# Optimization experiments

Hardware: AMD Instinct MI355X
Metric: run time of the kernel (lower is better)

Reference implementation:

```python
import jax, jax.numpy as jnp
import numpy as np
from jax.ops import segment_sum

N_NODES = 100_000
N_EDGES = 6_400_000
NUM_HOPS = 2
DECAY = 0.5
BC_INLET, BC_OUTLET, BC_WALL = 0.1, 0.0, 0.0


def setup_inputs() -> dict:
    key = jax.random.key(0)
    ks = jax.random.split(key, 12)
    pred = jax.random.normal(ks[0], (N_NODES,), jnp.float32)
    feats = jax.random.normal(ks[1], (N_NODES, 8), jnp.float32)
    b = jax.random.normal(ks[2], (N_NODES,), jnp.float32)
    vals = jax.random.normal(ks[3], (N_EDGES,), jnp.float32)
    ic_values = jax.random.normal(ks[4], (N_NODES,), jnp.float32)
    row_ptr = jnp.sort(jax.random.randint(ks[5], (N_NODES + 1,), 0, N_EDGES)).astype(jnp.int64)
    col_ind = jax.random.randint(ks[6], (N_EDGES,), 0, N_NODES).astype(jnp.int64)
    row_idx = jnp.sort(jax.random.randint(ks[7], (N_EDGES,), 0, N_NODES)).astype(jnp.int64)
    edge_index = jax.random.randint(ks[8], (2, N_EDGES), 0, N_NODES).astype(jnp.int64)
    ic_mask = jax.random.randint(ks[9], (N_NODES,), 0, 2) > 0
    inlet_mask = jax.random.randint(ks[10], (N_NODES,), 0, 2) > 0
    outlet_mask = jax.random.randint(ks[11], (N_NODES,), 0, 2) > 0
    wall_mask = jax.random.randint(jax.random.fold_in(key, 99), (N_NODES,), 0, 2) > 0
    return {"pred": pred, "feats": feats, "b": b, "vals": vals, "ic_values": ic_values,
            "row_ptr": row_ptr, "col_ind": col_ind, "row_idx": row_idx,
            "edge_index": edge_index, "ic_mask": ic_mask, "inlet_mask": inlet_mask,
            "outlet_mask": outlet_mask, "wall_mask": wall_mask, "epoch": 10}


def _masked_mse(pred, mask, target):
    m = mask.astype(pred.dtype)
    denom = jnp.maximum(m.sum(), 1.0)
    return jnp.sum(m * (pred - target) ** 2) / denom


def reference(pred, feats, b, vals, ic_values, row_ptr, col_ind, row_idx,
              edge_index, ic_mask, inlet_mask, outlet_mask, wall_mask, epoch):
    N = pred.shape[0]
    src, dst = edge_index[0], edge_index[1]

    # --- physics-based mesh-quality weight (edge-length-weighted gradient indicator) ---
    coords = feats[:, :2]                      # [N,2] node coordinates
    edge_len = jnp.sqrt(jnp.sum((coords[src] - coords[dst]) ** 2, axis=-1) + 1e-12)
    edge_grad = jnp.abs(pred[src] - pred[dst])
    quality = edge_len * edge_grad             # [E]
    ones_e = jnp.ones_like(quality)
    deg = jnp.maximum(segment_sum(ones_e, dst, num_segments=N), 1.0)
    w0 = 1.0 + segment_sum(quality, dst, num_segments=N) / deg
    w0 = w0 / jnp.mean(w0)

    # --- topology-aware multi-hop weight propagation ---
    w_cell = w0
    cur = w0
    for h in range(NUM_HOPS):
        cur = segment_sum(cur[src], dst, num_segments=N) / deg  # neighbor mean
        w_cell = w_cell + (DECAY ** (h + 1)) * cur

    # --- PDE residual: CSR (COO-expanded) sparse matvec ---
    Ax = segment_sum(vals * pred[col_ind], row_idx, num_segments=N)
    residual = Ax - b
    loss_pde = jnp.mean(w_cell * residual ** 2)

    # --- boundary condition losses ---
    loss_inlet = _masked_mse(pred, inlet_mask, BC_INLET)
    loss_outlet = _masked_mse(pred, outlet_mask, BC_OUTLET)
    loss_wall = _masked_mse(pred, wall_mask, BC_WALL)
    loss_bc = loss_inlet + loss_outlet + loss_wall

    # --- initial condition loss ---
    loss_ic = _masked_mse(pred, ic_mask, ic_values)

    # --- mass conservation: per-node net flux divergence ---
    flux = pred[src] - pred[dst]               # [E]
    net = segment_sum(flux, dst, num_segments=N)
    loss_cons = jnp.mean(net ** 2)

    # hierarchical adaptive lambdas reduce to 1.0 for a single forward pass
    loss_total = loss_pde + loss_bc + loss_ic + loss_cons
    return loss_total
```

## Files before the change

kernel.cpp:

```cpp
#include <hip/hip_runtime.h>

#define N_NODES 100000
#define N_EDGES 6400000

typedef unsigned long long u64;
typedef unsigned int u32;
typedef unsigned char u8;

#define QSCALE    8192.0f
#define QSCALE_INV (1.0 / 8192.0)
#define FLUXBIAS  12.0f
#define FSHIFT    26
#define CSHIFT    51

#define W_REGIONS   1024
#define EPW         6250
#define K_BUCKETS   256
#define RANGE       391
#define NPAD        100096
#define CAP         40
#define OVF_CAP     32768
#define OVB         8
#define SPLIT       8
#define CHUNK       (W_REGIONS / SPLIT)
#define AGG_BLOCKS  (K_BUCKETS * SPLIT + OVB)

#define EDGE_BLOCKS 6250
#define NBLK_NODE   391

enum { S_W0SUM = 0, S_CONS, S_IN_S, S_IN_C, S_OUT_S, S_OUT_C,
       S_WALL_S, S_WALL_C, S_IC_S, S_IC_C, S_PDE, S_NSLOT };
#define PS_STRIDE 16

__device__ __forceinline__ double wave_reduce(double v) {
    #pragma unroll
    for (int off = 32; off > 0; off >>= 1)
        v += __shfl_down(v, off, 64);
    return v;
}

__device__ __forceinline__ u64 edge_inc(float ps, float pd, float2 cs, float2 cd) {
    const float dx = cs.x - cd.x, dy = cs.y - cd.y;
    const float flux = ps - pd;
    const float q = sqrtf(dx * dx + dy * dy + 1e-12f) * fabsf(flux);
    const u64 qq = (u64)lrintf(fminf(q, 1024.0f) * QSCALE);
    const float fb = fminf(fmaxf(flux, -FLUXBIAS), FLUXBIAS) + FLUXBIAS;
    const u64 fq = (u64)lrintf(fb * QSCALE);
    return (1ull << CSHIFT) | (fq << FSHIFT) | qq;
}

__global__ __launch_bounds__(256) void shuffle_edges(
    const int* __restrict__ ei,
    u32* __restrict__ slab,
    u8* __restrict__ counts,
    u64* __restrict__ ovf,
    u32* __restrict__ ocnt)
{
    __shared__ u32 cur[K_BUCKETS];
    __shared__ u32 lslab[K_BUCKETS * CAP];
    for (int j = threadIdx.x; j < K_BUCKETS; j += 256) cur[j] = 0;
    __syncthreads();

    const int region = blockIdx.x;
    const int ebase = region * EPW;
    for (int k = threadIdx.x; k < EPW; k += 256) {
        const int e = ebase + k;
        const u32 s = (u32)ei[e];
        const u32 d = (u32)ei[N_EDGES + e];
        const u32 b = d / RANGE;
        const u32 dl = d - b * RANGE;
        const u32 pos = atomicAdd(&cur[b], 1u);
        if (pos < CAP) {
            lslab[b * CAP + pos] = (s << 9) | dl;
        } else {
            const u32 o = atomicAdd(ocnt, 1u);
            if (o < OVF_CAP) ovf[o] = ((u64)s << 32) | d;
        }
    }
    __syncthreads();
    const uint4* lsrc = (const uint4*)lslab;
    uint4* gdst = (uint4*)(slab + (size_t)region * K_BUCKETS * CAP);
    #pragma unroll
    for (int j = threadIdx.x; j < K_BUCKETS * CAP / 4; j += 256)
        gdst[j] = lsrc[j];
    for (int j = threadIdx.x; j < K_BUCKETS; j += 256)
        counts[region * K_BUCKETS + j] = (u8)min(cur[j], (u32)CAP);
}

__global__ __launch_bounds__(256) void agg_a(
    const u32* __restrict__ slab,
    const u8* __restrict__ counts,
    const u64* __restrict__ ovf,
    const u32* __restrict__ ocnt,
    const float* __restrict__ pred,
    const float* __restrict__ feats,
    u64* __restrict__ pk_part,
    u64* __restrict__ pk_ovf)
{
    if (blockIdx.x < K_BUCKETS * SPLIT) {
        __shared__ u64 acc[RANGE];
        for (int t = threadIdx.x; t < RANGE; t += 256) acc[t] = 0;
        __syncthreads();
        const int b = blockIdx.x >> 3;
        const int chunk = blockIdx.x & 7;
        const int wl = threadIdx.x >> 6, lane = threadIdx.x & 63;
        const int nbase = b * RANGE;
        for (int w = chunk * CHUNK + wl; w < (chunk + 1) * CHUNK; w += 4) {
            const int cnt = counts[w * K_BUCKETS + b];
            if (lane < cnt) {
                const u32 ent = slab[((size_t)w * K_BUCKETS + b) * CAP + lane];
                const int src = (int)(ent >> 9);
                const int dl = (int)(ent & 511u);
                const int d = nbase + dl;
                const float2 cs = *(const float2*)(feats + (size_t)src * 8);
                const float2 cd = *(const float2*)(feats + (size_t)d * 8);
                atomicAdd(&acc[dl], edge_inc(pred[src], pred[d], cs, cd));
            }
        }
        __syncthreads();
        for (int t = threadIdx.x; t < RANGE; t += 256)
            pk_part[(size_t)chunk * NPAD + nbase + t] = acc[t];
    } else {
        const int n = min((int)*ocnt, OVF_CAP);
        for (int o = (blockIdx.x - K_BUCKETS * SPLIT) * 256 + threadIdx.x;
             o < n; o += OVB * 256) {
            const u64 e = ovf[o];
            const int src = (int)(e >> 32);
            const int d = (int)(e & 0xffffffffu);
            const float2 cs = *(const float2*)(feats + (size_t)src * 8);
            const float2 cd = *(const float2*)(feats + (size_t)d * 8);
            atomicAdd(pk_ovf + d, edge_inc(pred[src], pred[d], cs, cd));
        }
    }
}

__global__ __launch_bounds__(256) void agg_hop(
    const u32* __restrict__ slab,
    const u8* __restrict__ counts,
    const u64* __restrict__ ovf,
    const u32* __restrict__ ocnt,
    const float* __restrict__ vsrc,
    float* __restrict__ hop_part,
    float* __restrict__ hop_ovf)
{
    if (blockIdx.x < K_BUCKETS * SPLIT) {
        __shared__ float acc[RANGE];
        for (int t = threadIdx.x; t < RANGE; t += 256) acc[t] = 0.0f;
        __syncthreads();
        const int b = blockIdx.x >> 3;
        const int chunk = blockIdx.x & 7;
        const int wl = threadIdx.x >> 6, lane = threadIdx.x & 63;
        const int nbase = b * RANGE;
        for (int w = chunk * CHUNK + wl; w < (chunk + 1) * CHUNK; w += 4) {
            const int cnt = counts[w * K_BUCKETS + b];
            if (lane < cnt) {
                const u32 ent = slab[((size_t)w * K_BUCKETS + b) * CAP + lane];
                atomicAdd(&acc[ent & 511u], vsrc[ent >> 9]);
            }
        }
        __syncthreads();
        for (int t = threadIdx.x; t < RANGE; t += 256)
            hop_part[(size_t)chunk * NPAD + nbase + t] = acc[t];
    } else {
        const int n = min((int)*ocnt, OVF_CAP);
        for (int o = (blockIdx.x - K_BUCKETS * SPLIT) * 256 + threadIdx.x;
             o < n; o += OVB * 256) {
            const u64 e = ovf[o];
            atomicAdd(hop_ovf + (int)(e & 0xffffffffu), vsrc[(int)(e >> 32)]);
        }
    }
}

__global__ __launch_bounds__(256) void ax_pass(
    const float* __restrict__ pred,
    const float* __restrict__ vals,
    const int* __restrict__ col_ind,
    const int* __restrict__ row_idx,
    float* __restrict__ Ax)
{
    const int stride = gridDim.x * blockDim.x;
    const unsigned lane = threadIdx.x & 63u;
    for (int e = blockIdx.x * blockDim.x + threadIdx.x; e < N_EDGES; e += stride) {
        const int r = row_idx[e];
        float av = vals[e] * pred[col_ind[e]];
        #pragma unroll
        for (int off = 1; off < 64; off <<= 1) {
            const float ov = __shfl_up(av, off, 64);
            const int   ok = __shfl_up(r,  off, 64);
            if ((int)lane >= off && ok == r) av += ov;
        }
        const int rn = __shfl_down(r, 1, 64);
        if (lane == 63u || rn != r) atomicAdd(Ax + r, av);
    }
}

__global__ __launch_bounds__(256) void edge_pass_a(
    const int* __restrict__ ei,
    const float* __restrict__ pred,
    const float* __restrict__ feats,
    const float* __restrict__ vals,
    const int* __restrict__ col_ind,
    const int* __restrict__ row_idx,
    u64* __restrict__ pk,
    float* __restrict__ Ax)
{
    const int stride = gridDim.x * blockDim.x;
    const unsigned lane = threadIdx.x & 63u;
    for (int e = blockIdx.x * blockDim.x + threadIdx.x; e < N_EDGES; e += stride) {
        const int s = ei[e];
        const int d = ei[N_EDGES + e];
        const float2 cs = *(const float2*)(feats + (size_t)s * 8);
        const float2 cd = *(const float2*)(feats + (size_t)d * 8);
        atomicAdd(pk + d, edge_inc(pred[s], pred[d], cs, cd));
        const int r = row_idx[e];
        float av = vals[e] * pred[col_ind[e]];
        #pragma unroll
        for (int off = 1; off < 64; off <<= 1) {
            const float ov = __shfl_up(av, off, 64);
            const int   ok = __shfl_up(r,  off, 64);
            if ((int)lane >= off && ok == r) av += ov;
        }
        const int rn = __shfl_down(r, 1, 64);
        if (lane == 63u || rn != r) atomicAdd(Ax + r, av);
    }
}

__global__ __launch_bounds__(256) void edge_hop(
    const int* __restrict__ ei,
    const float* __restrict__ srcval,
    float* __restrict__ accum)
{
    const int stride = gridDim.x * blockDim.x;
    for (int e = blockIdx.x * blockDim.x + threadIdx.x; e < N_EDGES; e += stride) {
        atomicAdd(accum + ei[N_EDGES + e], srcval[ei[e]]);
    }
}

__global__ __launch_bounds__(256) void node_b(
    const float* __restrict__ pred,
    const float* __restrict__ b,
    const float* __restrict__ ic_values,
    const int* __restrict__ inlet_mask,
    const int* __restrict__ outlet_mask,
    const int* __restrict__ wall_mask,
    const int* __restrict__ ic_mask,
    const u64* __restrict__ pk_part,
    const u64* __restrict__ pk_ovf,
    float* __restrict__ w0u_out,
    float* __restrict__ deg_out,
    float* __restrict__ Ax_res2,
    double* __restrict__ part_scal)
{
    const int i = blockIdx.x * blockDim.x + threadIdx.x;
    double v10[10];
    #pragma unroll
    for (int s = 0; s < 10; ++s) v10[s] = 0.0;
    if (i < N_NODES) {
        u64 v = pk_ovf[i];
        #pragma unroll
        for (int s2 = 0; s2 < SPLIT; ++s2) v += pk_part[(size_t)s2 * NPAD + i];
        const double cnt = (double)(v >> CSHIFT);
        const double qs  = (double)(v & ((1ull << FSHIFT) - 1)) * QSCALE_INV;
        const double fs  = (double)((v >> FSHIFT) & ((1ull << (CSHIFT - FSHIFT)) - 1)) * QSCALE_INV
                           - (double)FLUXBIAS * cnt;
        const float dg = fmaxf((float)cnt, 1.0f);
        deg_out[i] = dg;
        const float w = 1.0f + (float)qs / dg;
        w0u_out[i] = w;
        v10[S_W0SUM] = (double)w;
        v10[S_CONS] = fs * fs;
        const float p = pred[i];
        const float res = Ax_res2[i] - b[i];
        Ax_res2[i] = res * res;
        if (inlet_mask[i])  { const float t = p - 0.1f;         v10[S_IN_S]   = (double)t * t; v10[S_IN_C]   = 1.0; }
        if (outlet_mask[i]) {                                    v10[S_OUT_S]  = (double)p * p; v10[S_OUT_C]  = 1.0; }
        if (wall_mask[i])   {                                    v10[S_WALL_S] = (double)p * p; v10[S_WALL_C] = 1.0; }
        if (ic_mask[i])     { const float t = p - ic_values[i]; v10[S_IC_S]   = (double)t * t; v10[S_IC_C]   = 1.0; }
    }
    __shared__ double wred[4][10];
    const int wl = threadIdx.x >> 6, lane = threadIdx.x & 63;
    #pragma unroll
    for (int s = 0; s < 10; ++s) {
        const double r = wave_reduce(v10[s]);
        if (lane == 0) wred[wl][s] = r;
    }
    __syncthreads();
    if (threadIdx.x < 10) {
        const int s = threadIdx.x;
        part_scal[(size_t)blockIdx.x * PS_STRIDE + s] =
            wred[0][s] + wred[1][s] + wred[2][s] + wred[3][s];
    }
}

__global__ __launch_bounds__(256) void node_e(
    const float* __restrict__ hop_part,
    float* __restrict__ hop_ovf,
    const float* __restrict__ deg,
    float* __restrict__ cur1)
{
    const int i = blockIdx.x * blockDim.x + threadIdx.x;
    if (i < N_NODES) {
        float s = hop_ovf[i];
        #pragma unroll
        for (int s2 = 0; s2 < SPLIT; ++s2) s += hop_part[(size_t)s2 * NPAD + i];
        cur1[i] = s / deg[i];
        hop_ovf[i] = 0.0f;
    }
}

__global__ __launch_bounds__(256) void node_g(
    const float* __restrict__ w0u,
    const float* __restrict__ cur1,
    const float* __restrict__ hop_part,
    const float* __restrict__ hop_ovf,
    const float* __restrict__ deg,
    const float* __restrict__ res2,
    double* __restrict__ part_scal)
{
    const int i = blockIdx.x * blockDim.x + threadIdx.x;
    double pde = 0.0;
    if (i < N_NODES) {
        float nxt2 = hop_ovf[i];
        #pragma unroll
        for (int s2 = 0; s2 < SPLIT; ++s2) nxt2 += hop_part[(size_t)s2 * NPAD + i];
        const float w = w0u[i] + 0.5f * cur1[i] + 0.25f * (nxt2 / deg[i]);
        pde = (double)w * (double)res2[i];
    }
    __shared__ double wred[4];
    const int wl = threadIdx.x >> 6, lane = threadIdx.x & 63;
    const double r = wave_reduce(pde);
    if (lane == 0) wred[wl] = r;
    __syncthreads();
    if (threadIdx.x == 0)
        part_scal[(size_t)blockIdx.x * PS_STRIDE + S_PDE] =
            wred[0] + wred[1] + wred[2] + wred[3];
}

__global__ __launch_bounds__(256) void finalize(
    const double* __restrict__ part_scal, float* __restrict__ out)
{
    __shared__ double wred[4];
    __shared__ double res[S_NSLOT];
    const int wl = threadIdx.x >> 6, lane = threadIdx.x & 63;
    for (int s = 0; s < S_NSLOT; ++s) {
        double v = 0.0;
        for (int i = threadIdx.x; i < NBLK_NODE; i += 256)
            v += part_scal[(size_t)i * PS_STRIDE + s];
        v = wave_reduce(v);
        if (lane == 0) wred[wl] = v;
        __syncthreads();
        if (threadIdx.x == 0) res[s] = wred[0] + wred[1] + wred[2] + wred[3];
        __syncthreads();
    }
    if (threadIdx.x == 0) {
        const double pde = res[S_PDE] / res[S_W0SUM];
        const double bc  = res[S_IN_S]   / fmax(res[S_IN_C],   1.0)
                         + res[S_OUT_S]  / fmax(res[S_OUT_C],  1.0)
                         + res[S_WALL_S] / fmax(res[S_WALL_C], 1.0);
        const double ic  = res[S_IC_S] / fmax(res[S_IC_C], 1.0);
        const double cons = res[S_CONS] / (double)N_NODES;
        out[0] = (float)(pde + bc + ic + cons);
    }
}

extern "C" void kernel_launch(void* const* d_in, const int* in_sizes, int n_in,
                              void* d_out, int out_size, void* d_ws, size_t ws_size,
                              hipStream_t stream)
{
    const float* pred      = (const float*)d_in[0];
    const float* feats     = (const float*)d_in[1];
    const float* b         = (const float*)d_in[2];
    const float* vals      = (const float*)d_in[3];
    const float* ic_values = (const float*)d_in[4];
    const int* col_ind     = (const int*)d_in[6];
    const int* row_idx     = (const int*)d_in[7];
    const int* ei          = (const int*)d_in[8];
    const int* ic_mask     = (const int*)d_in[9];
    const int* inlet_mask  = (const int*)d_in[10];
    const int* outlet_mask = (const int*)d_in[11];
    const int* wall_mask   = (const int*)d_in[12];

    char* base = (char*)d_ws;
    float*  Ax       = (float*)base;
    u32*    ocnt     = (u32*)(base + 400000);
    u64*    pk_ovf   = (u64*)(base + 400128);
    float*  hop_ovf  = (float*)(base + 1200896);
    float*  w0u      = (float*)(base + 1601280);
    float*  deg      = (float*)(base + 2001280);
    float*  cur1     = (float*)(base + 2401280);
    double* part_scal= (double*)(base + 2801280);
    u64*    pk_part  = (u64*)(base + 2851328);
    float*  hop_part = (float*)(base + 9257472);
    u8*     counts   = (u8*)(base + 12460544);
    u64*    ovf      = (u64*)(base + 12722688);
    u32*    slab     = (u32*)(base + 12984832);
    const size_t needed = 12984832 + (size_t)W_REGIONS * K_BUCKETS * CAP * 4;

    const dim3 blk(256);
    const dim3 ngrid(NBLK_NODE);

    if (ws_size >= needed) {
        hipMemsetAsync(d_ws, 0, 1601280, stream);
        shuffle_edges<<<W_REGIONS, blk, 0, stream>>>(ei, slab, counts, ovf, ocnt);
        ax_pass<<<EDGE_BLOCKS, blk, 0, stream>>>(pred, vals, col_ind, row_idx, Ax);
        agg_a<<<AGG_BLOCKS, blk, 0, stream>>>(slab, counts, ovf, ocnt, pred, feats,
                                              pk_part, pk_ovf);
        node_b<<<ngrid, blk, 0, stream>>>(pred, b, ic_values,
                                          inlet_mask, outlet_mask, wall_mask, ic_mask,
                                          pk_part, pk_ovf, w0u, deg, Ax, part_scal);
        agg_hop<<<AGG_BLOCKS, blk, 0, stream>>>(slab, counts, ovf, ocnt, w0u,
                                                hop_part, hop_ovf);
        node_e<<<ngrid, blk, 0, stream>>>(hop_part, hop_ovf, deg, cur1);
        agg_hop<<<AGG_BLOCKS, blk, 0, stream>>>(slab, counts, ovf, ocnt, cur1,
                                                hop_part, hop_ovf);
        node_g<<<ngrid, blk, 0, stream>>>(w0u, cur1, hop_part, hop_ovf, deg, Ax,
                                          part_scal);
    } else {
        hipMemsetAsync(d_ws, 0, 12460544, stream);
        const dim3 egrid(EDGE_BLOCKS);
        edge_pass_a<<<egrid, blk, 0, stream>>>(ei, pred, feats, vals, col_ind, row_idx,
                                               pk_ovf, Ax);
        node_b<<<ngrid, blk, 0, stream>>>(pred, b, ic_values,
                                          inlet_mask, outlet_mask, wall_mask, ic_mask,
                                          pk_part, pk_ovf, w0u, deg, Ax, part_scal);
        edge_hop<<<egrid, blk, 0, stream>>>(ei, w0u, hop_ovf);
        node_e<<<ngrid, blk, 0, stream>>>(hop_part, hop_ovf, deg, cur1);
        edge_hop<<<egrid, blk, 0, stream>>>(ei, cur1, hop_ovf);
        node_g<<<ngrid, blk, 0, stream>>>(w0u, cur1, hop_part, hop_ovf, deg, Ax,
                                          part_scal);
    }
    finalize<<<1, blk, 0, stream>>>(part_scal, (float*)d_out);
}
```

Before: 446.5 us.

## Compact bucket entries via prefix scan and stage destination node data in LDS

The aggregation kernels used to give each wavefront one region slot and mask lanes past that slot's count, so about 24 of 64 lanes sat idle when each slot holds roughly 24 edges. The new code builds a shared-memory prefix sum of per-region counts, and each thread binary-searches its segment, so threads stay densely busy across all entries. agg_a also preloads the destination nodes' pred values and coordinates into LDS, so the per-edge gather of destination data leaves global memory. The cost is a scan with several barriers per block and a 7-step binary search per edge, and slab reads are less contiguous per wavefront.

Measured after the change: 410.0 us. 1.09x faster.

```diff
diff --git a/kernel.cpp b/kernel.cpp
--- a/kernel.cpp
+++ b/kernel.cpp
@@ -87,6 +87,36 @@
         counts[region * K_BUCKETS + j] = (u8)min(cur[j], (u32)CAP);
 }
 
+__device__ __forceinline__ void build_prefix(
+    const u8* __restrict__ counts, int b, int chunk, u32* pref)
+{
+    if (threadIdx.x < CHUNK)
+        pref[threadIdx.x + 1] = counts[(chunk * CHUNK + threadIdx.x) * K_BUCKETS + b];
+    if (threadIdx.x == 0) pref[0] = 0;
+    __syncthreads();
+    for (int off = 1; off < CHUNK; off <<= 1) {
+        u32 v = 0;
+        if (threadIdx.x < CHUNK) {
+            const int idx = threadIdx.x + 1;
+            v = pref[idx] + ((idx - off >= 1) ? pref[idx - off] : 0u);
+        }
+        __syncthreads();
+        if (threadIdx.x < CHUNK) pref[threadIdx.x + 1] = v;
+        __syncthreads();
+    }
+}
+
+__device__ __forceinline__ int find_seg(const u32* pref, int k)
+{
+    int lo = 0, hi = CHUNK;
+    #pragma unroll
+    for (int it = 0; it < 7; ++it) {
+        const int mid = (lo + hi) >> 1;
+        if (pref[mid] <= (u32)k) lo = mid; else hi = mid;
+    }
+    return lo;
+}
+
 __global__ __launch_bounds__(256) void agg_a(
     const u32* __restrict__ slab,
     const u8* __restrict__ counts,
@@ -99,23 +129,33 @@
 {
     if (blockIdx.x < K_BUCKETS * SPLIT) {
         __shared__ u64 acc[RANGE];
-        for (int t = threadIdx.x; t < RANGE; t += 256) acc[t] = 0;
-        __syncthreads();
+        __shared__ u32 pref[CHUNK + 1];
+        __shared__ float  pred_l[RANGE];
+        __shared__ float2 coord_l[RANGE];
         const int b = blockIdx.x >> 3;
         const int chunk = blockIdx.x & 7;
-        const int wl = threadIdx.x >> 6, lane = threadIdx.x & 63;
         const int nbase = b * RANGE;
-        for (int w = chunk * CHUNK + wl; w < (chunk + 1) * CHUNK; w += 4) {
-            const int cnt = counts[w * K_BUCKETS + b];
-            if (lane < cnt) {
-                const u32 ent = slab[((size_t)w * K_BUCKETS + b) * CAP + lane];
-                const int src = (int)(ent >> 9);
-                const int dl = (int)(ent & 511u);
-                const int d = nbase + dl;
-                const float2 cs = *(const float2*)(feats + (size_t)src * 8);
-                const float2 cd = *(const float2*)(feats + (size_t)d * 8);
-                atomicAdd(&acc[dl], edge_inc(pred[src], pred[d], cs, cd));
+        for (int t = threadIdx.x; t < RANGE; t += 256) {
+            acc[t] = 0;
+            const int node = nbase + t;
+            if (node < N_NODES) {
+                pred_l[t] = pred[node];
+                coord_l[t] = *(const float2*)(feats + (size_t)node * 8);
+            } else {
+                pred_l[t] = 0.0f; coord_l[t] = make_float2(0.0f, 0.0f);
             }
+        }
+        build_prefix(counts, b, chunk, pref);
+        const int total = (int)pref[CHUNK];
+        for (int k = threadIdx.x; k < total; k += 256) {
+            const int seg = find_seg(pref, k);
+            const int w = chunk * CHUNK + seg;
+            const int slot = k - (int)pref[seg];
+            const u32 ent = slab[((size_t)w * K_BUCKETS + b) * CAP + slot];
+            const int src = (int)(ent >> 9);
+            const int dl = (int)(ent & 511u);
+            const float2 cs = *(const float2*)(feats + (size_t)src * 8);
+            atomicAdd(&acc[dl], edge_inc(pred[src], pred_l[dl], cs, coord_l[dl]));
         }
         __syncthreads();
         for (int t = threadIdx.x; t < RANGE; t += 256)
@@ -145,18 +185,19 @@
 {
     if (blockIdx.x < K_BUCKETS * SPLIT) {
         __shared__ float acc[RANGE];
-        for (int t = threadIdx.x; t < RANGE; t += 256) acc[t] = 0.0f;
-        __syncthreads();
+        __shared__ u32 pref[CHUNK + 1];
         const int b = blockIdx.x >> 3;
         const int chunk = blockIdx.x & 7;
-        const int wl = threadIdx.x >> 6, lane = threadIdx.x & 63;
         const int nbase = b * RANGE;
-        for (int w = chunk * CHUNK + wl; w < (chunk + 1) * CHUNK; w += 4) {
-            const int cnt = counts[w * K_BUCKETS + b];
-            if (lane < cnt) {
-                const u32 ent = slab[((size_t)w * K_BUCKETS + b) * CAP + lane];
-                atomicAdd(&acc[ent & 511u], vsrc[ent >> 9]);
-            }
+        for (int t = threadIdx.x; t < RANGE; t += 256) acc[t] = 0.0f;
+        build_prefix(counts, b, chunk, pref);
+        const int total = (int)pref[CHUNK];
+        for (int k = threadIdx.x; k < total; k += 256) {
+            const int seg = find_seg(pref, k);
+            const int w = chunk * CHUNK + seg;
+            const int slot = k - (int)pref[seg];
+            const u32 ent = slab[((size_t)w * K_BUCKETS + b) * CAP + slot];
+            atomicAdd(&acc[ent & 511u], vsrc[ent >> 9]);
         }
         __syncthreads();
         for (int t = threadIdx.x; t < RANGE; t += 256)
```
